# Kernel optimization log

Measured on AMD Instinct MI355X. Metric: run time of the kernel, lower is better.

The kernel has to match this reference:

```python
import jax, jax.numpy as jnp
import numpy as np

DIM = 2048
N_HEADS = 16
N_KV_HEADS = 4
HEAD_DIM = DIM // N_HEADS  # 128
N_REP = N_HEADS // N_KV_HEADS
MAX_SEQ_LEN = 4096
SEQLEN = 4096


def setup_inputs() -> dict:
    key = jax.random.key(0)
    ks = jax.random.split(key, 6)
    x = jax.random.normal(ks[0], (1, SEQLEN, DIM), dtype=jnp.float32)
    # rotary frequencies, llama-style theta=10000
    inv_freq = 1.0 / (10000.0 ** (np.arange(0, HEAD_DIM, 2, dtype=np.float32) / HEAD_DIM))
    t = np.arange(SEQLEN, dtype=np.float32)
    ang = np.outer(t, inv_freq)  # [S, head_dim/2]
    freqs_cos = jnp.asarray(np.cos(ang))
    freqs_sin = jnp.asarray(np.sin(ang))
    # additive causal mask [S, S]
    mask = jnp.where(jnp.tril(jnp.ones((SEQLEN, SEQLEN), dtype=bool)), 0.0, -1e9).astype(jnp.float32)
    sc = 0.02
    wq = jax.random.normal(ks[1], (DIM, N_HEADS * HEAD_DIM), dtype=jnp.float32) * sc
    wk = jax.random.normal(ks[2], (DIM, N_KV_HEADS * HEAD_DIM), dtype=jnp.float32) * sc
    wv = jax.random.normal(ks[3], (DIM, N_KV_HEADS * HEAD_DIM), dtype=jnp.float32) * sc
    wo = jax.random.normal(ks[4], (N_HEADS * HEAD_DIM, DIM), dtype=jnp.float32) * sc
    return {"x": x, "start_pos": 0, "freqs_cos": freqs_cos, "freqs_sin": freqs_sin,
            "mask": mask, "wq": wq, "wk": wk, "wv": wv, "wo": wo}


def _rope(x, cos, sin):
    # x: [b, s, h, d]; cos/sin: [s, d/2]; consecutive pairs form complex numbers
    b, s, h, d = x.shape
    xr = x.astype(jnp.float32).reshape(b, s, h, d // 2, 2)
    x1, x2 = xr[..., 0], xr[..., 1]
    c = cos[None, :, None, :]
    sn = sin[None, :, None, :]
    o1 = x1 * c - x2 * sn
    o2 = x1 * sn + x2 * c
    return jnp.stack([o1, o2], axis=-1).reshape(b, s, h, d).astype(x.dtype)


def reference(x, start_pos, freqs_cos, freqs_sin, mask, wq, wk, wv, wo):
    bsz, seqlen, _ = x.shape
    xq = (x @ wq).reshape(bsz, seqlen, N_HEADS, HEAD_DIM)
    xk = (x @ wk).reshape(bsz, seqlen, N_KV_HEADS, HEAD_DIM)
    xv = (x @ wv).reshape(bsz, seqlen, N_KV_HEADS, HEAD_DIM)
    xq = _rope(xq, freqs_cos, freqs_sin)
    xk = _rope(xk, freqs_cos, freqs_sin)
    # KV-cache append (cache is zeros before this call)
    cache_k = jnp.zeros((1, MAX_SEQ_LEN, N_KV_HEADS, HEAD_DIM), dtype=xk.dtype)
    cache_v = jnp.zeros((1, MAX_SEQ_LEN, N_KV_HEADS, HEAD_DIM), dtype=xv.dtype)
    cache_k = jax.lax.dynamic_update_slice(cache_k, xk, (0, start_pos, 0, 0))
    cache_v = jax.lax.dynamic_update_slice(cache_v, xv, (0, start_pos, 0, 0))
    keys = cache_k[:bsz, : start_pos + seqlen]    # [b, T, kvh, d]
    values = cache_v[:bsz, : start_pos + seqlen]
    # GQA repeat to full head count
    keys = jnp.repeat(keys, N_REP, axis=2)
    values = jnp.repeat(values, N_REP, axis=2)
    scale = 1.0 / jnp.sqrt(jnp.float32(HEAD_DIM))
    scores = jnp.einsum('bshd,bthd->bhst', xq, keys) * scale  # [b, h, s, T]
    scores = scores + mask[None, None, :, :]
    probs = jax.nn.softmax(scores.astype(jnp.float32), axis=-1).astype(xq.dtype)
    out = jnp.einsum('bhst,bthd->bshd', probs, values).reshape(bsz, seqlen, -1)
    return out @ wo
```

## Files before the change

kernel.cpp:

```cpp
#include <hip/hip_runtime.h>
#include <hip/hip_bf16.h>
#include <stdint.h>

#define SEQ 4096
#define DIM 2048
#define NH 16
#define NKV 4
#define HD 128
#define KVLD 1024


using frag8 = __attribute__((ext_vector_type(8))) short;
using f32x4 = __attribute__((ext_vector_type(4))) float;

union VecU { ushort u[8]; uint4 v; };

__device__ __forceinline__ float bf2f(ushort u) {
    union { uint32_t u; float f; } v; v.u = ((uint32_t)u) << 16; return v.f;
}
__device__ __forceinline__ ushort f2bf(float f) {
    union { float f; uint32_t u; } v; v.f = f;
    uint32_t r = v.u + 0x7fffu + ((v.u >> 16) & 1u);
    return (ushort)(r >> 16);
}

__device__ __forceinline__ void glds16(const void* g, void* l) {
    __builtin_amdgcn_global_load_lds(
        (const __attribute__((address_space(1))) void*)g,
        (__attribute__((address_space(3))) void*)l, 16, 0, 0);
}

__global__ __launch_bounds__(256) void prep_kernel(
    const float* __restrict__ x, const float* __restrict__ wq,
    const float* __restrict__ wk, const float* __restrict__ wv,
    ushort* __restrict__ Xb, ushort* __restrict__ WqT, ushort* __restrict__ KVT)
{
    __shared__ ushort T[32][36];
    int b = blockIdx.x;
    if (b < 4096) {
        size_t i = ((size_t)b * 256 + threadIdx.x) * 8;
        float4 f0 = *(const float4*)&x[i];
        float4 f1 = *(const float4*)&x[i + 4];
        VecU t;
        t.u[0] = f2bf(f0.x); t.u[1] = f2bf(f0.y); t.u[2] = f2bf(f0.z); t.u[3] = f2bf(f0.w);
        t.u[4] = f2bf(f1.x); t.u[5] = f2bf(f1.y); t.u[6] = f2bf(f1.z); t.u[7] = f2bf(f1.w);
        *(uint4*)&Xb[i] = t.v;
    } else {
        const int K = DIM;
        int v  = b - 4096;
        int bx = v % 96;
        int by = v / 96;
        const float* src; ushort* dst; int N, bn;
        if (bx < 64)      { src = wq; dst = WqT;                     N = DIM; bn = bx * 32; }
        else if (bx < 80) { src = wk; dst = KVT;                     N = 512; bn = (bx - 64) * 32; }
        else              { src = wv; dst = KVT + (size_t)512 * DIM; N = 512; bn = (bx - 80) * 32; }
        int r  = threadIdx.x >> 3;
        int c4 = (threadIdx.x & 7) * 4;
        int bk = by * 32;
        float4 w = *(const float4*)&src[(size_t)(bk + r) * N + bn + c4];
        T[r][c4]     = f2bf(w.x); T[r][c4 + 1] = f2bf(w.y);
        T[r][c4 + 2] = f2bf(w.z); T[r][c4 + 3] = f2bf(w.w);
        __syncthreads();
        ushort4 o;
        o.x = T[c4][r]; o.y = T[c4 + 1][r]; o.z = T[c4 + 2][r]; o.w = T[c4 + 3][r];
        *(ushort4*)&dst[(size_t)(bn + r) * K + bk + c4] = o;
    }
}

__global__ __launch_bounds__(256) void fuse3_kernel(
    ushort* __restrict__ Qb, ushort* __restrict__ KVb, ushort* __restrict__ VT,
    const float* __restrict__ Cos, const float* __restrict__ Sin)
{
    __shared__ ushort T[32][36];
    int b = blockIdx.x;
    if (b < 20480) {
        ushort* X; int log2nh, strideT, idx; float osc;
        if (b < 16384) { X = Qb;  log2nh = 4; strideT = DIM;  osc = 0.08838834764831845f; idx = b * 256 + threadIdx.x; }
        else           { X = KVb; log2nh = 2; strideT = KVLD; osc = 1.0f; idx = (b - 16384) * 256 + threadIdx.x; }
        int p = idx & 63;
        int h = (idx >> 6) & ((1 << log2nh) - 1);
        int t = idx >> (6 + log2nh);
        size_t base = (size_t)t * strideT + (size_t)h * 128 + 2 * p;
        ushort2 xv = *(ushort2*)&X[base];
        float x1 = bf2f(xv.x), x2 = bf2f(xv.y);
        float c = Cos[t * 64 + p], s = Sin[t * 64 + p];
        ushort2 ov;
        ov.x = f2bf((x1 * c - x2 * s) * osc);
        ov.y = f2bf((x1 * s + x2 * c) * osc);
        *(ushort2*)&X[base] = ov;
    } else {
        int v  = b - 20480;
        int bd = (v & 15) * 32;
        int bt = (v >> 4) * 32;
        int r  = threadIdx.x >> 3;
        int c4 = (threadIdx.x & 7) * 4;
        ushort4 w = *(const ushort4*)&KVb[(size_t)(bt + r) * KVLD + 512 + bd + c4];
        T[r][c4] = w.x; T[r][c4 + 1] = w.y; T[r][c4 + 2] = w.z; T[r][c4 + 3] = w.w;
        __syncthreads();
        ushort4 o;
        o.x = T[c4][r]; o.y = T[c4 + 1][r]; o.z = T[c4 + 2][r]; o.w = T[c4 + 3][r];
        *(ushort4*)&VT[(size_t)(bd + r) * SEQ + bt + c4] = o;
    }
}

template <int CF>
__global__ __launch_bounds__(256) void gemm_tn(
    const ushort* __restrict__ A, const ushort* __restrict__ BT,
    void* __restrict__ C, int M, int N, int K)
{
    __shared__ ushort As[128 * 32];
    __shared__ ushort Bs[128 * 32];

    const int tid  = threadIdx.x;
    const int lane = tid & 63;
    const int wave = tid >> 6;
    const int bm   = blockIdx.y * 128;
    const int bn   = blockIdx.x * 128;
    const int wm   = (wave >> 1) * 64;
    const int wn   = (wave & 1) * 64;
    const int quad = lane >> 4;
    const int t16  = lane & 15;
    const int kg   = quad ^ ((t16 >> 1) & 3);

    f32x4 acc[4][4] = {};

    for (int k0 = 0; k0 < K; k0 += 32) {
        #pragma unroll
        for (int it = 0; it < 2; ++it) {
            int gid = it * 256 + tid;
            int r   = gid >> 2;
            int cs  = (gid & 3) ^ ((gid >> 3) & 3);
            glds16(&A[(size_t)(bm + r) * K + k0 + cs * 8],
                   &As[(it * 256 + wave * 64) * 8]);
            glds16(&BT[(size_t)(bn + r) * K + k0 + cs * 8],
                   &Bs[(it * 256 + wave * 64) * 8]);
        }
        __syncthreads();

        frag8 af[4], bf[4];
        #pragma unroll
        for (int i = 0; i < 4; ++i)
            af[i] = *(const frag8*)&As[(wm + i * 16 + t16) * 32 + kg * 8];
        #pragma unroll
        for (int j = 0; j < 4; ++j)
            bf[j] = *(const frag8*)&Bs[(wn + j * 16 + t16) * 32 + kg * 8];
        #pragma unroll
        for (int i = 0; i < 4; ++i)
            #pragma unroll
            for (int j = 0; j < 4; ++j)
                acc[i][j] = __builtin_amdgcn_mfma_f32_16x16x32_bf16(
                    af[i], bf[j], acc[i][j], 0, 0, 0);
        __syncthreads();
    }

    #pragma unroll
    for (int i = 0; i < 4; ++i)
        #pragma unroll
        for (int j = 0; j < 4; ++j)
            #pragma unroll
            for (int r = 0; r < 4; ++r) {
                int row = bm + wm + i * 16 + quad * 4 + r;
                int col = bn + wn + j * 16 + t16;
                if (CF) ((float*)C)[(size_t)row * N + col] = acc[i][j][r];
                else    ((ushort*)C)[(size_t)row * N + col] = f2bf(acc[i][j][r]);
            }
}

__global__ __launch_bounds__(256) void gemm_qkv(
    const ushort* __restrict__ A, const ushort* __restrict__ BT,
    ushort* __restrict__ Cq, ushort* __restrict__ Ckv)
{
    const int K = DIM;
    __shared__ ushort As[128 * 32];
    __shared__ ushort Bs[128 * 32];

    const int tid  = threadIdx.x;
    const int lane = tid & 63;
    const int wave = tid >> 6;
    const int bm   = blockIdx.y * 128;
    const int bn   = blockIdx.x * 128;
    const int wm   = (wave >> 1) * 64;
    const int wn   = (wave & 1) * 64;
    const int quad = lane >> 4;
    const int t16  = lane & 15;
    const int kg   = quad ^ ((t16 >> 1) & 3);

    f32x4 acc[4][4] = {};

    for (int k0 = 0; k0 < K; k0 += 32) {
        #pragma unroll
        for (int it = 0; it < 2; ++it) {
            int gid = it * 256 + tid;
            int r   = gid >> 2;
            int cs  = (gid & 3) ^ ((gid >> 3) & 3);
            glds16(&A[(size_t)(bm + r) * K + k0 + cs * 8],
                   &As[(it * 256 + wave * 64) * 8]);
            glds16(&BT[(size_t)(bn + r) * K + k0 + cs * 8],
                   &Bs[(it * 256 + wave * 64) * 8]);
        }
        __syncthreads();

        frag8 af[4], bf[4];
        #pragma unroll
        for (int i = 0; i < 4; ++i)
            af[i] = *(const frag8*)&As[(wm + i * 16 + t16) * 32 + kg * 8];
        #pragma unroll
        for (int j = 0; j < 4; ++j)
            bf[j] = *(const frag8*)&Bs[(wn + j * 16 + t16) * 32 + kg * 8];
        #pragma unroll
        for (int i = 0; i < 4; ++i)
            #pragma unroll
            for (int j = 0; j < 4; ++j)
                acc[i][j] = __builtin_amdgcn_mfma_f32_16x16x32_bf16(
                    af[i], bf[j], acc[i][j], 0, 0, 0);
        __syncthreads();
    }

    ushort* C;
    int ldc, cb;
    if (bn < 2048) { C = Cq;  ldc = DIM;  cb = 0; }
    else           { C = Ckv; ldc = KVLD; cb = 2048; }

    #pragma unroll
    for (int i = 0; i < 4; ++i)
        #pragma unroll
        for (int j = 0; j < 4; ++j)
            #pragma unroll
            for (int r = 0; r < 4; ++r) {
                int row = bm + wm + i * 16 + quad * 4 + r;
                int col = bn + wn + j * 16 + t16;
                C[(size_t)row * ldc + (col - cb)] = f2bf(acc[i][j][r]);
            }
}

__global__ __launch_bounds__(256, 2) void attn_kernel(
    const ushort* __restrict__ Q, const ushort* __restrict__ Kb,
    const ushort* __restrict__ VT, ushort* __restrict__ Oab,
    ushort* __restrict__ Oev, float2* __restrict__ lmE, float2* __restrict__ lmO)
{
    __shared__ ushort Ks[64][136];
    __shared__ ushort Vt[128][72];
    __shared__ ushort Sp[4][32][72];

    const int tid  = threadIdx.x;
    const int lane = tid & 63;
    const int wave = tid >> 6;
    const int quad = lane >> 4;
    const int t16  = lane & 15;
    const int hp   = blockIdx.x;
    const int hA   = 2 * hp;
    const int hB   = 2 * hp + 1;
    const int kvh  = hp >> 1;

    frag8 vONE;
    #pragma unroll
    for (int i = 0; i < 8; ++i) vONE[i] = (short)0x3F80;

    const int by = (int)blockIdx.y;
    int qt, c, split;
    if (by < 64) { split = 1; qt = 63 - (by >> 1); c = by & 1; }
    else         { split = 0; qt = 95 - by;        c = 0;      }
    const int n  = qt + 1;
    const int q0 = qt * 64;
    const int qwave = q0 + wave * 16;
    const int qmaxw = qwave + 15;
    const int tstart = (split && c) ? (n / 2) * 64 : 0;
    const int tend   = (split && !c) ? (n / 2) * 64 : n * 64;

    frag8 aQA[4], aQB[4];
    #pragma unroll
    for (int kk = 0; kk < 4; ++kk) {
        aQA[kk] = *(const frag8*)&Q[(size_t)(qwave + t16) * DIM + hA * HD + kk * 32 + quad * 8];
        aQB[kk] = *(const frag8*)&Q[(size_t)(qwave + t16) * DIM + hB * HD + kk * 32 + quad * 8];
    }

    f32x4 oA[8] = {}, oB[8] = {};
    f32x4 o9A = {0.f, 0.f, 0.f, 0.f};
    f32x4 o9B = {0.f, 0.f, 0.f, 0.f};
    float mA[4] = {0.f, 0.f, 0.f, 0.f};
    float mB[4] = {0.f, 0.f, 0.f, 0.f};

    for (int t0 = tstart; t0 < tend; t0 += 64) {
        #pragma unroll
        for (int it = 0; it < 4; ++it) {
            int idx = tid + it * 256;
            int tt  = idx >> 4;
            int cc  = (idx & 15) * 8;
            *(uint4*)&Ks[tt][cc] =
                *(const uint4*)&Kb[(size_t)(t0 + tt) * KVLD + kvh * HD + cc];
        }
        #pragma unroll
        for (int it = 0; it < 4; ++it) {
            int idx = tid + it * 256;
            int d   = idx >> 3;
            int tq  = (idx & 7) * 8;
            *(uint4*)&Vt[d][tq] =
                *(const uint4*)&VT[(size_t)(kvh * HD + d) * SEQ + t0 + tq];
        }
        __syncthreads();

        const bool hi = (t0 + 32 <= qmaxw);

        f32x4 sA0 = {0.f,0.f,0.f,0.f}, sA1 = {0.f,0.f,0.f,0.f};
        f32x4 sA2 = {0.f,0.f,0.f,0.f}, sA3 = {0.f,0.f,0.f,0.f};
        f32x4 sB0 = {0.f,0.f,0.f,0.f}, sB1 = {0.f,0.f,0.f,0.f};
        f32x4 sB2 = {0.f,0.f,0.f,0.f}, sB3 = {0.f,0.f,0.f,0.f};

        __builtin_amdgcn_s_setprio(1);
        #pragma unroll
        for (int kk = 0; kk < 4; ++kk) {
            frag8 b0 = *(const frag8*)&Ks[2 * t16][kk * 32 + quad * 8];
            frag8 b1 = *(const frag8*)&Ks[2 * t16 + 1][kk * 32 + quad * 8];
            sA0 = __builtin_amdgcn_mfma_f32_16x16x32_bf16(aQA[kk], b0, sA0, 0, 0, 0);
            sB0 = __builtin_amdgcn_mfma_f32_16x16x32_bf16(aQB[kk], b0, sB0, 0, 0, 0);
            sA1 = __builtin_amdgcn_mfma_f32_16x16x32_bf16(aQA[kk], b1, sA1, 0, 0, 0);
            sB1 = __builtin_amdgcn_mfma_f32_16x16x32_bf16(aQB[kk], b1, sB1, 0, 0, 0);
        }
        if (hi) {
            #pragma unroll
            for (int kk = 0; kk < 4; ++kk) {
                frag8 b2 = *(const frag8*)&Ks[32 + 2 * t16][kk * 32 + quad * 8];
                frag8 b3 = *(const frag8*)&Ks[33 + 2 * t16][kk * 32 + quad * 8];
                sA2 = __builtin_amdgcn_mfma_f32_16x16x32_bf16(aQA[kk], b2, sA2, 0, 0, 0);
                sB2 = __builtin_amdgcn_mfma_f32_16x16x32_bf16(aQB[kk], b2, sB2, 0, 0, 0);
                sA3 = __builtin_amdgcn_mfma_f32_16x16x32_bf16(aQA[kk], b3, sA3, 0, 0, 0);
                sB3 = __builtin_amdgcn_mfma_f32_16x16x32_bf16(aQB[kk], b3, sB3, 0, 0, 0);
            }
        }
        __builtin_amdgcn_s_setprio(0);

        const bool mLo = (t0 + 31 > qwave);
        const bool mHi = (t0 + 63 > qwave);

        bool trig = false;
        #pragma unroll
        for (int r = 0; r < 4; ++r) {
            int q = qwave + quad * 4 + r;
            bool x0 = mLo && (t0 + 2 * t16 > q);
            bool x1 = mLo && (t0 + 2 * t16 + 1 > q);
            bool x2 = mHi && (t0 + 32 + 2 * t16 > q);
            bool x3 = mHi && (t0 + 33 + 2 * t16 > q);
            float vA0 = x0 ? -30000.f : sA0[r];
            float vA1 = x1 ? -30000.f : sA1[r];
            float vA2 = (hi && !x2) ? sA2[r] : -30000.f;
            float vA3 = (hi && !x3) ? sA3[r] : -30000.f;
            float vB0 = x0 ? -30000.f : sB0[r];
            float vB1 = x1 ? -30000.f : sB1[r];
            float vB2 = (hi && !x2) ? sB2[r] : -30000.f;
            float vB3 = (hi && !x3) ? sB3[r] : -30000.f;
            float lmA = fmaxf(fmaxf(vA0, vA1), fmaxf(vA2, vA3));
            float lmB = fmaxf(fmaxf(vB0, vB1), fmaxf(vB2, vB3));
            trig |= (lmA > mA[r] + 8.f) | (lmB > mB[r] + 8.f);
            float eA0 = __expf(vA0 - mA[r]);
            float eA1 = __expf(vA1 - mA[r]);
            float eB0 = __expf(vB0 - mB[r]);
            float eB1 = __expf(vB1 - mB[r]);
            *(uint*)&Sp[wave][quad * 4 + r][2 * t16] =
                (uint)f2bf(eA0) | ((uint)f2bf(eA1) << 16);
            *(uint*)&Sp[wave][16 + quad * 4 + r][2 * t16] =
                (uint)f2bf(eB0) | ((uint)f2bf(eB1) << 16);
            if (hi) {
                float eA2 = __expf(vA2 - mA[r]);
                float eA3 = __expf(vA3 - mA[r]);
                float eB2 = __expf(vB2 - mB[r]);
                float eB3 = __expf(vB3 - mB[r]);
                *(uint*)&Sp[wave][quad * 4 + r][32 + 2 * t16] =
                    (uint)f2bf(eA2) | ((uint)f2bf(eA3) << 16);
                *(uint*)&Sp[wave][16 + quad * 4 + r][32 + 2 * t16] =
                    (uint)f2bf(eB2) | ((uint)f2bf(eB3) << 16);
            }
        }

        if (__any(trig)) {
            #pragma unroll
            for (int r = 0; r < 4; ++r) {
                int q = qwave + quad * 4 + r;
                bool x0 = mLo && (t0 + 2 * t16 > q);
                bool x1 = mLo && (t0 + 2 * t16 + 1 > q);
                bool x2 = mHi && (t0 + 32 + 2 * t16 > q);
                bool x3 = mHi && (t0 + 33 + 2 * t16 > q);
                float vA0 = x0 ? -30000.f : sA0[r];
                float vA1 = x1 ? -30000.f : sA1[r];
                float vA2 = (hi && !x2) ? sA2[r] : -30000.f;
                float vA3 = (hi && !x3) ? sA3[r] : -30000.f;
                float vB0 = x0 ? -30000.f : sB0[r];
                float vB1 = x1 ? -30000.f : sB1[r];
                float vB2 = (hi && !x2) ? sB2[r] : -30000.f;
                float vB3 = (hi && !x3) ? sB3[r] : -30000.f;
                float rmA = fmaxf(fmaxf(vA0, vA1), fmaxf(vA2, vA3));
                float rmB = fmaxf(fmaxf(vB0, vB1), fmaxf(vB2, vB3));
                rmA = fmaxf(rmA, __shfl_xor(rmA, 1));
                rmA = fmaxf(rmA, __shfl_xor(rmA, 2));
                rmA = fmaxf(rmA, __shfl_xor(rmA, 4));
                rmA = fmaxf(rmA, __shfl_xor(rmA, 8));
                rmB = fmaxf(rmB, __shfl_xor(rmB, 1));
                rmB = fmaxf(rmB, __shfl_xor(rmB, 2));
                rmB = fmaxf(rmB, __shfl_xor(rmB, 4));
                rmB = fmaxf(rmB, __shfl_xor(rmB, 8));
                float mnA = fmaxf(mA[r], rmA);
                float mnB = fmaxf(mB[r], rmB);
                float alA = __expf(mA[r] - mnA);
                float alB = __expf(mB[r] - mnB);
                #pragma unroll
                for (int j = 0; j < 8; ++j) { oA[j][r] *= alA; oB[j][r] *= alB; }
                o9A[r] *= alA; o9B[r] *= alB;
                mA[r] = mnA; mB[r] = mnB;
                float eA0 = __expf(vA0 - mnA);
                float eA1 = __expf(vA1 - mnA);
                float eB0 = __expf(vB0 - mnB);
                float eB1 = __expf(vB1 - mnB);
                *(uint*)&Sp[wave][quad * 4 + r][2 * t16] =
                    (uint)f2bf(eA0) | ((uint)f2bf(eA1) << 16);
                *(uint*)&Sp[wave][16 + quad * 4 + r][2 * t16] =
                    (uint)f2bf(eB0) | ((uint)f2bf(eB1) << 16);
                if (hi) {
                    float eA2 = __expf(vA2 - mnA);
                    float eA3 = __expf(vA3 - mnA);
                    float eB2 = __expf(vB2 - mnB);
                    float eB3 = __expf(vB3 - mnB);
                    *(uint*)&Sp[wave][quad * 4 + r][32 + 2 * t16] =
                        (uint)f2bf(eA2) | ((uint)f2bf(eA3) << 16);
                    *(uint*)&Sp[wave][16 + quad * 4 + r][32 + 2 * t16] =
                        (uint)f2bf(eB2) | ((uint)f2bf(eB3) << 16);
                }
            }
        }

        frag8 aPA0 = *(const frag8*)&Sp[wave][t16][quad * 8];
        frag8 aPB0 = *(const frag8*)&Sp[wave][16 + t16][quad * 8];
        __builtin_amdgcn_s_setprio(1);
        #pragma unroll
        for (int j = 0; j < 8; ++j) {
            frag8 bV = *(const frag8*)&Vt[j * 16 + t16][quad * 8];
            oA[j] = __builtin_amdgcn_mfma_f32_16x16x32_bf16(aPA0, bV, oA[j], 0, 0, 0);
            oB[j] = __builtin_amdgcn_mfma_f32_16x16x32_bf16(aPB0, bV, oB[j], 0, 0, 0);
        }
        o9A = __builtin_amdgcn_mfma_f32_16x16x32_bf16(aPA0, vONE, o9A, 0, 0, 0);
        o9B = __builtin_amdgcn_mfma_f32_16x16x32_bf16(aPB0, vONE, o9B, 0, 0, 0);
        if (hi) {
            frag8 aPA1 = *(const frag8*)&Sp[wave][t16][32 + quad * 8];
            frag8 aPB1 = *(const frag8*)&Sp[wave][16 + t16][32 + quad * 8];
            #pragma unroll
            for (int j = 0; j < 8; ++j) {
                frag8 bV = *(const frag8*)&Vt[j * 16 + t16][32 + quad * 8];
                oA[j] = __builtin_amdgcn_mfma_f32_16x16x32_bf16(aPA1, bV, oA[j], 0, 0, 0);
                oB[j] = __builtin_amdgcn_mfma_f32_16x16x32_bf16(aPB1, bV, oB[j], 0, 0, 0);
            }
            o9A = __builtin_amdgcn_mfma_f32_16x16x32_bf16(aPA1, vONE, o9A, 0, 0, 0);
            o9B = __builtin_amdgcn_mfma_f32_16x16x32_bf16(aPB1, vONE, o9B, 0, 0, 0);
        }
        __builtin_amdgcn_s_setprio(0);
        __syncthreads();
    }

    if (split) {
        ushort* dst = c ? Oab : Oev;
        float2* lm  = c ? lmO : lmE;
        #pragma unroll
        for (int r = 0; r < 4; ++r) {
            int row = qwave + quad * 4 + r;
            if (t16 == 0) {
                lm[(size_t)(row - 2048) * NH + hA] = make_float2(o9A[r], mA[r]);
                lm[(size_t)(row - 2048) * NH + hB] = make_float2(o9B[r], mB[r]);
            }
            #pragma unroll
            for (int j = 0; j < 8; ++j) {
                dst[(size_t)row * DIM + hA * HD + j * 16 + t16] = f2bf(oA[j][r]);
                dst[(size_t)row * DIM + hB * HD + j * 16 + t16] = f2bf(oB[j][r]);
            }
        }
    } else {
        #pragma unroll
        for (int r = 0; r < 4; ++r) {
            float invA = 1.f / fmaxf(o9A[r], 1e-20f);
            float invB = 1.f / fmaxf(o9B[r], 1e-20f);
            int row = qwave + quad * 4 + r;
            #pragma unroll
            for (int j = 0; j < 8; ++j) {
                Oab[(size_t)row * DIM + hA * HD + j * 16 + t16] = f2bf(oA[j][r] * invA);
                Oab[(size_t)row * DIM + hB * HD + j * 16 + t16] = f2bf(oB[j][r] * invB);
            }
        }
    }
}

__global__ __launch_bounds__(256) void post_kernel(
    const ushort* __restrict__ oE, const ushort* __restrict__ oO,
    const float2* __restrict__ lmE, const float2* __restrict__ lmO,
    ushort* __restrict__ out, const float* __restrict__ wo,
    ushort* __restrict__ WoT)
{
    __shared__ ushort T[32][36];
    int b = blockIdx.x;
    if (b < 2048) {
        size_t e = (size_t)(SEQ / 2) * DIM + ((size_t)b * 256 + threadIdx.x) * 8;
        int row = (int)(e >> 11);
        int h   = (int)((e >> 7) & 15);
        float2 LE = lmE[(size_t)(row - 2048) * NH + h];
        float2 LO = lmO[(size_t)(row - 2048) * NH + h];
        float ms = fmaxf(LE.y, LO.y);
        float aE = __expf(LE.y - ms);
        float aO = __expf(LO.y - ms);
        float inv = 1.f / fmaxf(LE.x * aE + LO.x * aO, 1e-20f);
        aE *= inv; aO *= inv;
        VecU uE, uO, uR;
        uE.v = *(const uint4*)&oE[e];
        uO.v = *(const uint4*)&oO[e];
        #pragma unroll
        for (int j = 0; j < 8; ++j)
            uR.u[j] = f2bf(bf2f(uE.u[j]) * aE + bf2f(uO.u[j]) * aO);
        *(uint4*)&out[e] = uR.v;
    } else {
        int v  = b - 2048;
        int bn = (v & 63) * 32;
        int bk = (v >> 6) * 32;
        int r  = threadIdx.x >> 3;
        int c4 = (threadIdx.x & 7) * 4;
        float4 w = *(const float4*)&wo[(size_t)(bk + r) * DIM + bn + c4];
        T[r][c4]     = f2bf(w.x); T[r][c4 + 1] = f2bf(w.y);
        T[r][c4 + 2] = f2bf(w.z); T[r][c4 + 3] = f2bf(w.w);
        __syncthreads();
        ushort4 o;
        o.x = T[c4][r]; o.y = T[c4 + 1][r]; o.z = T[c4 + 2][r]; o.w = T[c4 + 3][r];
        *(ushort4*)&WoT[(size_t)(bn + r) * DIM + bk + c4] = o;
    }
}

extern "C" void kernel_launch(void* const* d_in, const int* in_sizes, int n_in,
                              void* d_out, int out_size, void* d_ws, size_t ws_size,
                              hipStream_t stream)
{
    const float* x  = (const float*)d_in[0];
    const float* fc = (const float*)d_in[2];
    const float* fs = (const float*)d_in[3];
    const float* wq = (const float*)d_in[5];
    const float* wk = (const float*)d_in[6];
    const float* wv = (const float*)d_in[7];
    const float* wo = (const float*)d_in[8];

    ushort* Qb  = (ushort*)d_ws;
    ushort* KVb = Qb + (size_t)SEQ * DIM;
    ushort* Ab  = KVb + (size_t)SEQ * KVLD;
    ushort* WqT = Ab;
    ushort* KVT = Ab + (size_t)DIM * DIM;
    ushort* WoT = KVb;

    ushort* Xb = (ushort*)d_out;
    ushort* VT = Xb + (size_t)SEQ * DIM;
    float2* lmE = (float2*)(VT + (size_t)512 * SEQ);
    float2* lmO = lmE + (size_t)(SEQ / 2) * NH;

    dim3 blk(256);

    prep_kernel<<<4096 + 96 * 64, blk, 0, stream>>>(x, wq, wk, wv, Xb, WqT, KVT);

    gemm_qkv<<<dim3(3072 / 128, SEQ / 128), blk, 0, stream>>>(Xb, Ab, Qb, KVb);

    fuse3_kernel<<<16384 + 4096 + 2048, blk, 0, stream>>>(Qb, KVb, VT, fc, fs);

    attn_kernel<<<dim3(NH / 2, 96), blk, 0, stream>>>(
        Qb, KVb, VT, Ab, Xb, lmE, lmO);

    post_kernel<<<2048 + 64 * 64, blk, 0, stream>>>(
        Xb, Ab, lmE, lmO, Ab, wo, WoT);

    gemm_tn<1><<<dim3(DIM / 128, SEQ / 128), blk, 0, stream>>>(Ab, WoT, d_out, SEQ, DIM, DIM);
}
```

Baseline: 430.1 us.

## Read K and V fragments directly from global memory in attention kernel

Removes the shared-memory staging of K and V tiles in the attention kernel. Each wave now loads its MFMA B-fragments straight from global memory, and the block-wide barriers go away. The launch-bounds occupancy hint is dropped. This trades away LDS traffic and synchronisation for repeated global/L2 reads, since the four waves each fetch the same K/V data. Loads also become latency-exposed with no explicit prefetch.

```diff
diff --git a/kernel.cpp b/kernel.cpp
--- a/kernel.cpp
+++ b/kernel.cpp
@@ -233,13 +233,11 @@
             }
 }
 
-__global__ __launch_bounds__(256, 2) void attn_kernel(
+__global__ __launch_bounds__(256) void attn_kernel(
     const ushort* __restrict__ Q, const ushort* __restrict__ Kb,
     const ushort* __restrict__ VT, ushort* __restrict__ Oab,
     ushort* __restrict__ Oev, float2* __restrict__ lmE, float2* __restrict__ lmO)
 {
-    __shared__ ushort Ks[64][136];
-    __shared__ ushort Vt[128][72];
     __shared__ ushort Sp[4][32][72];
 
     const int tid  = threadIdx.x;
@@ -267,6 +265,9 @@
     const int tstart = (split && c) ? (n / 2) * 64 : 0;
     const int tend   = (split && !c) ? (n / 2) * 64 : n * 64;
 
+    const ushort* Kh = Kb + (size_t)kvh * HD;
+    const ushort* Vh = VT + (size_t)(kvh * HD) * SEQ;
+
     frag8 aQA[4], aQB[4];
     #pragma unroll
     for (int kk = 0; kk < 4; ++kk) {
@@ -281,24 +282,6 @@
     float mB[4] = {0.f, 0.f, 0.f, 0.f};
 
     for (int t0 = tstart; t0 < tend; t0 += 64) {
-        #pragma unroll
-        for (int it = 0; it < 4; ++it) {
-            int idx = tid + it * 256;
-            int tt  = idx >> 4;
-            int cc  = (idx & 15) * 8;
-            *(uint4*)&Ks[tt][cc] =
-                *(const uint4*)&Kb[(size_t)(t0 + tt) * KVLD + kvh * HD + cc];
-        }
-        #pragma unroll
-        for (int it = 0; it < 4; ++it) {
-            int idx = tid + it * 256;
-            int d   = idx >> 3;
-            int tq  = (idx & 7) * 8;
-            *(uint4*)&Vt[d][tq] =
-                *(const uint4*)&VT[(size_t)(kvh * HD + d) * SEQ + t0 + tq];
-        }
-        __syncthreads();
-
         const bool hi = (t0 + 32 <= qmaxw);
 
         f32x4 sA0 = {0.f,0.f,0.f,0.f}, sA1 = {0.f,0.f,0.f,0.f};
@@ -309,8 +292,8 @@
         __builtin_amdgcn_s_setprio(1);
         #pragma unroll
         for (int kk = 0; kk < 4; ++kk) {
-            frag8 b0 = *(const frag8*)&Ks[2 * t16][kk * 32 + quad * 8];
-            frag8 b1 = *(const frag8*)&Ks[2 * t16 + 1][kk * 32 + quad * 8];
+            frag8 b0 = *(const frag8*)&Kh[(size_t)(t0 + 2 * t16) * KVLD + kk * 32 + quad * 8];
+            frag8 b1 = *(const frag8*)&Kh[(size_t)(t0 + 2 * t16 + 1) * KVLD + kk * 32 + quad * 8];
             sA0 = __builtin_amdgcn_mfma_f32_16x16x32_bf16(aQA[kk], b0, sA0, 0, 0, 0);
             sB0 = __builtin_amdgcn_mfma_f32_16x16x32_bf16(aQB[kk], b0, sB0, 0, 0, 0);
             sA1 = __builtin_amdgcn_mfma_f32_16x16x32_bf16(aQA[kk], b1, sA1, 0, 0, 0);
@@ -319,8 +302,8 @@
         if (hi) {
             #pragma unroll
             for (int kk = 0; kk < 4; ++kk) {
-                frag8 b2 = *(const frag8*)&Ks[32 + 2 * t16][kk * 32 + quad * 8];
-                frag8 b3 = *(const frag8*)&Ks[33 + 2 * t16][kk * 32 + quad * 8];
+                frag8 b2 = *(const frag8*)&Kh[(size_t)(t0 + 32 + 2 * t16) * KVLD + kk * 32 + quad * 8];
+                frag8 b3 = *(const frag8*)&Kh[(size_t)(t0 + 33 + 2 * t16) * KVLD + kk * 32 + quad * 8];
                 sA2 = __builtin_amdgcn_mfma_f32_16x16x32_bf16(aQA[kk], b2, sA2, 0, 0, 0);
                 sB2 = __builtin_amdgcn_mfma_f32_16x16x32_bf16(aQB[kk], b2, sB2, 0, 0, 0);
                 sA3 = __builtin_amdgcn_mfma_f32_16x16x32_bf16(aQA[kk], b3, sA3, 0, 0, 0);
@@ -431,7 +414,7 @@
         __builtin_amdgcn_s_setprio(1);
         #pragma unroll
         for (int j = 0; j < 8; ++j) {
-            frag8 bV = *(const frag8*)&Vt[j * 16 + t16][quad * 8];
+            frag8 bV = *(const frag8*)&Vh[(size_t)(j * 16 + t16) * SEQ + t0 + quad * 8];
             oA[j] = __builtin_amdgcn_mfma_f32_16x16x32_bf16(aPA0, bV, oA[j], 0, 0, 0);
             oB[j] = __builtin_amdgcn_mfma_f32_16x16x32_bf16(aPB0, bV, oB[j], 0, 0, 0);
         }
@@ -442,7 +425,7 @@
             frag8 aPB1 = *(const frag8*)&Sp[wave][16 + t16][32 + quad * 8];
             #pragma unroll
             for (int j = 0; j < 8; ++j) {
-                frag8 bV = *(const frag8*)&Vt[j * 16 + t16][32 + quad * 8];
+                frag8 bV = *(const frag8*)&Vh[(size_t)(j * 16 + t16) * SEQ + t0 + 32 + quad * 8];
                 oA[j] = __builtin_amdgcn_mfma_f32_16x16x32_bf16(aPA1, bV, oA[j], 0, 0, 0);
                 oB[j] = __builtin_amdgcn_mfma_f32_16x16x32_bf16(aPB1, bV, oB[j], 0, 0, 0);
             }
@@ -450,7 +433,6 @@
             o9B = __builtin_amdgcn_mfma_f32_16x16x32_bf16(aPB1, vONE, o9B, 0, 0, 0);
         }
         __builtin_amdgcn_s_setprio(0);
-        __syncthreads();
     }
 
     if (split) {
```

New measurement: 698.6 us. 62.4% more time.
